# Kernel tuning notes

Measured on AMD Instinct MI355X. Metric: run time of the kernel, lower is better.

Reference implementation:

```python
import jax, jax.numpy as jnp
import numpy as np

N_NODES = 50000
N_EDGES = 800000
NODE_IN = 16
NODE_OUT = 3
H = 128
N_LAYERS = 3


def setup_inputs() -> dict:
    key = jax.random.key(0)
    ks = jax.random.split(key, 16)
    s = 0.05
    inp = {
        "x": jax.random.normal(ks[0], (N_NODES, NODE_IN), dtype=jnp.float32),
        "edge_index": jax.random.randint(ks[1], (2, N_EDGES), 0, N_NODES, dtype=jnp.int64),
        # encoder / decoder
        "enc_w": jax.random.normal(ks[2], (NODE_IN, H), dtype=jnp.float32) * s,
        "enc_b": jnp.zeros((H,), dtype=jnp.float32),
        "dec_w": jax.random.normal(ks[3], (H, NODE_OUT), dtype=jnp.float32) * s,
        "dec_b": jnp.zeros((NODE_OUT,), dtype=jnp.float32),
        # 3 processor layers, edge MLP: Linear(2H,H) -> ReLU -> Linear(H,H)
        "edge_w1": jax.random.normal(ks[4], (N_LAYERS, 2 * H, H), dtype=jnp.float32) * s,
        "edge_b1": jnp.zeros((N_LAYERS, H), dtype=jnp.float32),
        "edge_w2": jax.random.normal(ks[5], (N_LAYERS, H, H), dtype=jnp.float32) * s,
        "edge_b2": jnp.zeros((N_LAYERS, H), dtype=jnp.float32),
        # node MLP: Linear(2H,H) -> ReLU -> Linear(H,H)
        "node_w1": jax.random.normal(ks[6], (N_LAYERS, 2 * H, H), dtype=jnp.float32) * s,
        "node_b1": jnp.zeros((N_LAYERS, H), dtype=jnp.float32),
        "node_w2": jax.random.normal(ks[7], (N_LAYERS, H, H), dtype=jnp.float32) * s,
        "node_b2": jnp.zeros((N_LAYERS, H), dtype=jnp.float32),
    }
    return inp


def reference(x, edge_index, enc_w, enc_b, dec_w, dec_b,
              edge_w1, edge_b1, edge_w2, edge_b2,
              node_w1, node_b1, node_w2, node_b2):
    row = edge_index[0]  # source nodes
    col = edge_index[1]  # destination nodes
    h = x @ enc_w + enc_b  # [N, H]
    for l in range(N_LAYERS):
        # EdgeModel: cat(src, dest) -> MLP
        e_in = jnp.concatenate([h[row], h[col]], axis=1)  # [E, 2H]
        e = jnp.maximum(e_in @ edge_w1[l] + edge_b1[l], 0.0) @ edge_w2[l] + edge_b2[l]  # [E, H]
        # NodeModel: scatter_add messages by col, cat with x -> MLP
        agg = jax.ops.segment_sum(e, col, num_segments=h.shape[0])  # [N, H]
        n_in = jnp.concatenate([h, agg], axis=1)  # [N, 2H]
        h_upd = jnp.maximum(n_in @ node_w1[l] + node_b1[l], 0.0) @ node_w2[l] + node_b2[l]
        h = h + h_upd  # residual
    return h @ dec_w + dec_b  # [N, NODE_OUT]
```

## Files before the change

### kernel.cpp

```cpp
#include <hip/hip_runtime.h>
#include <hip/hip_bf16.h>
#include <stdint.h>

#define N_NODES 50000
#define N_EDGES 800000
#define HID 128
#define NODE_IN 16
#define NODE_OUT 3
#define EDGE_TILES 12500
#define NODE_TILES 782
#define SCAN_BLOCKS 196

typedef __attribute__((ext_vector_type(8))) short short8;
typedef __attribute__((ext_vector_type(4))) float f32x4;

__device__ __forceinline__ unsigned short f2bf(float f) {
    union { float f; unsigned int u; } v; v.f = f;
    unsigned int u = v.u;
    u += 0x7fff + ((u >> 16) & 1);
    return (unsigned short)(u >> 16);
}
__device__ __forceinline__ float bf2f(unsigned short s) {
    union { unsigned int u; float f; } v; v.u = ((unsigned int)s) << 16;
    return v.f;
}
__device__ __forceinline__ float bfu_lo(unsigned int u) {
    union { unsigned int u; float f; } v; v.u = u << 16; return v.f;
}
__device__ __forceinline__ float bfu_hi(unsigned int u) {
    union { unsigned int u; float f; } v; v.u = u & 0xffff0000u; return v.f;
}

__global__ void k1_hist_mfold(const int* __restrict__ colp, int* __restrict__ cnt,
                              int* __restrict__ rank,
                              const float* __restrict__ edge_w2, const float* __restrict__ node_w1,
                              const float* __restrict__ edge_b2,
                              float* __restrict__ Mtmp, float* __restrict__ Vtmp) {
    for (int e = blockIdx.x * 256 + threadIdx.x; e < N_EDGES; e += gridDim.x * 256)
        rank[e] = atomicAdd(&cnt[colp[e]], 1);
    for (int d = blockIdx.x * 256 + threadIdx.x; d < 3 * 16384; d += gridDim.x * 256) {
        int L = d / 16384, rem = d & 16383;
        int k = rem >> 7, n = rem & 127;
        const float* w2  = edge_w2 + (size_t)L * 16384;
        const float* w1b = node_w1 + (size_t)L * 32768 + 16384;
        float acc = 0.f;
        #pragma unroll 4
        for (int j = 0; j < 128; j++) acc += w2[k * 128 + j] * w1b[j * 128 + n];
        Mtmp[d] = acc;
        if (k == 0) {
            const float* b2 = edge_b2 + (size_t)L * 128;
            float vv = 0.f;
            #pragma unroll 4
            for (int j = 0; j < 128; j++) vv += b2[j] * w1b[j * 128 + n];
            Vtmp[L * 128 + n] = vv;
        }
    }
}

__global__ __launch_bounds__(256) void k2a_scan1_swizzle(
    const int* __restrict__ cnt, int* __restrict__ ex, int* __restrict__ bsums,
    const float* __restrict__ edge_w1, const float* __restrict__ node_w1,
    const float* __restrict__ node_w2, const float* __restrict__ Mtmp,
    unsigned short* __restrict__ swz) {
    __shared__ int s[256];
    int b = blockIdx.x, t = threadIdx.x;
    if (b < SCAN_BLOCKS) {
        int i = b * 256 + t;
        int v = (i < N_NODES) ? cnt[i] : 0;
        s[t] = v;
        __syncthreads();
        for (int off = 1; off < 256; off <<= 1) {
            int u = (t >= off) ? s[t - off] : 0;
            __syncthreads();
            s[t] += u;
            __syncthreads();
        }
        if (i < N_NODES) ex[i] = s[t] - v;
        if (t == 255) bsums[b] = s[255];
    } else {
        for (int d = (b - SCAN_BLOCKS) * 256 + t; d < 3 * 98304;
             d += (gridDim.x - SCAN_BLOCKS) * 256) {
            int L = d / 98304;
            int rem = d - L * 98304;
            unsigned short* base = swz + L * 98304;
            if (rem < 32768) {
                const float* w1 = edge_w1 + (size_t)L * 32768;
                int j = rem & 7, ll = (rem >> 3) & 63, tt = rem >> 9;
                int nt = tt & 15, kt = tt >> 4;
                int k = kt * 32 + ((ll >> 4) << 3) + j;
                int cc = nt * 16 + (ll & 15);
                float v = (cc < 128) ? w1[k * 128 + cc] : w1[(128 + k) * 128 + (cc - 128)];
                base[rem] = f2bf(v);
            } else if (rem < 49152) {
            } else if (rem < 81920) {
                int d2 = rem - 49152;
                int j = d2 & 7, ll = (d2 >> 3) & 63, tt = d2 >> 9;
                int nt = tt & 7, kt = tt >> 3;
                int k = kt * 32 + ((ll >> 4) << 3) + j, n = (nt << 4) + (ll & 15);
                float v = (k < 128) ? node_w1[(size_t)L * 32768 + k * 128 + n]
                                    : Mtmp[(size_t)L * 16384 + (k - 128) * 128 + n];
                base[rem] = f2bf(v);
            } else {
                int d2 = rem - 81920;
                const float* src = node_w2 + (size_t)L * 16384;
                int j = d2 & 7, ll = (d2 >> 3) & 63, tt = d2 >> 9;
                int nt = tt & 7, kt = tt >> 3;
                int k = kt * 32 + ((ll >> 4) << 3) + j, n = (nt << 4) + (ll & 15);
                base[rem] = f2bf(src[k * 128 + n]);
            }
        }
    }
}

__global__ __launch_bounds__(256) void k3a_scatter(
    const int* __restrict__ rowp, const int* __restrict__ colp,
    const int* __restrict__ ex, const int* __restrict__ bsums,
    const int* __restrict__ rank, int2* __restrict__ rc_sorted) {
    __shared__ int sc[256];
    __shared__ int ls[SCAN_BLOCKS];
    int t = threadIdx.x;
    int v = (t < SCAN_BLOCKS) ? bsums[t] : 0;
    sc[t] = v;
    __syncthreads();
    for (int off = 1; off < 256; off <<= 1) {
        int u = (t >= off) ? sc[t - off] : 0;
        __syncthreads();
        sc[t] += u;
        __syncthreads();
    }
    if (t < SCAN_BLOCKS) ls[t] = sc[t] - v;
    __syncthreads();

    int e = blockIdx.x * 256 + t;
    if (e >= N_EDGES) return;
    int c = colp[e];
    int pos = ex[c] + ls[c >> 8] + rank[e];
    rc_sorted[pos] = make_int2(rowp[e], c);
}

__global__ __launch_bounds__(256, 4) void k3b_encoder_sd(
    const float* __restrict__ x, const float* __restrict__ enc_w, const float* __restrict__ enc_b,
    const unsigned short* __restrict__ w1c, unsigned short* __restrict__ h,
    unsigned short* __restrict__ S, unsigned short* __restrict__ D, float* __restrict__ aggH)
{
    __shared__ float wts[NODE_IN * HID];
    __shared__ float bts[HID];
    __shared__ float xs[64][NODE_IN];
    __shared__ unsigned short hs[64][136];
    int t = threadIdx.x, wave = t >> 6, l = t & 63, q = l >> 4, l16 = l & 15;
    int n0 = blockIdx.x * 64;
    int nt0s = wave * 4;

    for (int i = t; i < NODE_IN * HID; i += 256) wts[i] = enc_w[i];
    if (t < HID) bts[t] = enc_b[t];
    for (int i = t; i < 64 * NODE_IN; i += 256) {
        int nl = i >> 4, ii = i & 15;
        int n = n0 + nl;
        xs[nl][ii] = (n < N_NODES) ? x[n * NODE_IN + ii] : 0.f;
    }
    for (int o = t; o < 64 * 32; o += 256) {
        int nl = o >> 5, c4 = o & 31;
        int n = n0 + nl;
        if (n < N_NODES) *(f32x4*)&aggH[n * HID + c4 * 4] = (f32x4){0.f, 0.f, 0.f, 0.f};
    }
    short8 wr[4][4];
    #pragma unroll
    for (int kt = 0; kt < 4; kt++)
        #pragma unroll
        for (int i = 0; i < 4; i++)
            wr[kt][i] = *(const short8*)(w1c + ((kt * 16 + nt0s + i) * 64 + l) * 8);
    __syncthreads();

    for (int o = t; o < 64 * HID; o += 256) {
        int nl = o >> 7, cc = o & 127;
        float acc = bts[cc];
        #pragma unroll
        for (int i = 0; i < NODE_IN; i++) acc += xs[nl][i] * wts[i * HID + cc];
        unsigned short hb = f2bf(acc);
        hs[nl][cc] = hb;
        int n = n0 + nl;
        if (n < N_NODES) h[n * HID + cc] = hb;
    }
    __syncthreads();

    f32x4 acc[4][4];
    #pragma unroll
    for (int g = 0; g < 4; g++)
        #pragma unroll
        for (int i = 0; i < 4; i++) acc[g][i] = (f32x4){0.f, 0.f, 0.f, 0.f};
    #pragma unroll
    for (int kt = 0; kt < 4; kt++) {
        #pragma unroll
        for (int g = 0; g < 4; g++) {
            short8 a = *(const short8*)&hs[g * 16 + l16][kt * 32 + q * 8];
            #pragma unroll
            for (int i = 0; i < 4; i++)
                acc[g][i] = __builtin_amdgcn_mfma_f32_16x16x32_bf16(a, wr[kt][i], acc[g][i], 0, 0, 0);
        }
    }
    #pragma unroll
    for (int i = 0; i < 4; i++) {
        int cc = (nt0s + i) * 16 + l16;
        #pragma unroll
        for (int g = 0; g < 4; g++)
            #pragma unroll
            for (int r = 0; r < 4; r++) {
                int n = n0 + g * 16 + q * 4 + r;
                if (n < N_NODES) {
                    unsigned short v = f2bf(acc[g][i][r]);
                    if (cc < 128) S[n * HID + cc] = v;
                    else          D[n * HID + (cc - 128)] = v;
                }
            }
    }
}

__global__ __launch_bounds__(256, 8) void edge_kernel(
    const unsigned short* __restrict__ S, const unsigned short* __restrict__ D,
    const int2* __restrict__ rc_sorted,
    const float* __restrict__ b1, float* __restrict__ aggH)
{
    __shared__ unsigned short hid_s[64][136];
    __shared__ int row_s[64], col_s[64];
    int t = threadIdx.x;
    int ch = t & 15;

    float b1v[8];
    #pragma unroll
    for (int j = 0; j < 8; j++) b1v[j] = b1[ch * 8 + j];

    for (int tile = blockIdx.x; tile < EDGE_TILES; tile += gridDim.x) {
        int e0 = tile * 64;
        if (t < 64) {
            int2 rc = rc_sorted[e0 + t];
            row_s[t] = rc.x;
            col_s[t] = rc.y;
        }
        __syncthreads();

        #pragma unroll
        for (int it = 0; it < 4; it++) {
            int el = it * 16 + (t >> 4);
            int r = row_s[el], c = col_s[el];
            short8 sv = *(const short8*)(S + (size_t)r * HID + ch * 8);
            short8 dv = *(const short8*)(D + (size_t)c * HID + ch * 8);
            short8 o;
            #pragma unroll
            for (int p = 0; p < 4; p++) {
                unsigned int us = ((const unsigned int*)&sv)[p];
                unsigned int ud = ((const unsigned int*)&dv)[p];
                float v0 = bfu_lo(us) + bfu_lo(ud) + b1v[p * 2];
                float v1 = bfu_hi(us) + bfu_hi(ud) + b1v[p * 2 + 1];
                ((unsigned short*)&o)[p * 2]     = f2bf(v0 > 0.f ? v0 : 0.f);
                ((unsigned short*)&o)[p * 2 + 1] = f2bf(v1 > 0.f ? v1 : 0.f);
            }
            *(short8*)&hid_s[el][ch * 8] = o;
        }
        __syncthreads();

        {
            int c = t & 127;
            int h2 = t >> 7;
            int r0 = h2 * 32;
            float accv = 0.f;
            int cur = col_s[r0];
            #pragma unroll 4
            for (int r = r0; r < r0 + 32; r++) {
                accv += bf2f(hid_s[r][c]);
                int nxt = (r == r0 + 31) ? -1 : col_s[r + 1];
                if (nxt != cur) {
                    unsafeAtomicAdd(&aggH[cur * HID + c], accv);
                    accv = 0.f;
                    cur = nxt;
                }
            }
        }
        __syncthreads();
    }
}

template<int LAST>
__global__ __launch_bounds__(256, 4) void node_kernel(
    unsigned short* __restrict__ h, float* __restrict__ aggH, const int* __restrict__ cnt,
    const unsigned short* __restrict__ w1m_s, const float* __restrict__ b1,
    const float* __restrict__ vfold,
    const unsigned short* __restrict__ w2s, const float* __restrict__ b2,
    const unsigned short* __restrict__ w1c_next,
    unsigned short* __restrict__ S, unsigned short* __restrict__ D,
    const float* __restrict__ dec_w, const float* __restrict__ dec_b, float* __restrict__ out)
{
    __shared__ unsigned short in_h[64][136];
    __shared__ unsigned short in_a[64][136];
    __shared__ int cnt_s[64];
    __shared__ float dw[HID * NODE_OUT];
    __shared__ float db[NODE_OUT];
    int t = threadIdx.x, wave = t >> 6, l = t & 63, q = l >> 4, l16 = l & 15;
    int nt0 = wave * 2, nt0s = wave * 4;
    int n0 = blockIdx.x * 64;

    if (LAST) {
        for (int i = t; i < HID * NODE_OUT; i += 256) dw[i] = dec_w[i];
        if (t < NODE_OUT) db[t] = dec_b[t];
    }

    #pragma unroll
    for (int it = 0; it < 8; it++) {
        int g = it * 256 + t;
        int nl = g >> 5, sub = g & 31, half = sub >> 4, li = sub & 15;
        int n = n0 + nl;
        short8 v = (short8){0, 0, 0, 0, 0, 0, 0, 0};
        if (n < N_NODES) {
            if (half == 0) {
                v = *(const short8*)(h + n * HID + li * 8);
            } else {
                float* ap = aggH + n * HID + li * 8;
                f32x4 a0 = *(f32x4*)ap, a1 = *(f32x4*)(ap + 4);
                #pragma unroll
                for (int j = 0; j < 4; j++) {
                    ((unsigned short*)&v)[j]     = f2bf(a0[j]);
                    ((unsigned short*)&v)[4 + j] = f2bf(a1[j]);
                }
                if (!LAST) {
                    *(f32x4*)ap       = (f32x4){0.f, 0.f, 0.f, 0.f};
                    *(f32x4*)(ap + 4) = (f32x4){0.f, 0.f, 0.f, 0.f};
                }
            }
        }
        if (half == 0) *(short8*)&in_h[nl][li * 8] = v;
        else           *(short8*)&in_a[nl][li * 8] = v;
    }
    if (t < 64) cnt_s[t] = (n0 + t < N_NODES) ? cnt[n0 + t] : 0;
    __syncthreads();

    float b1r0 = b1[nt0 * 16 + l16], b1r1 = b1[(nt0 + 1) * 16 + l16];
    float vr0 = vfold[nt0 * 16 + l16], vr1 = vfold[(nt0 + 1) * 16 + l16];
    float b2r0 = b2[nt0 * 16 + l16], b2r1 = b2[(nt0 + 1) * 16 + l16];

    f32x4 acc[4][2];
    #pragma unroll
    for (int g = 0; g < 4; g++)
        #pragma unroll
        for (int j = 0; j < 2; j++) acc[g][j] = (f32x4){0.f, 0.f, 0.f, 0.f};
    #pragma unroll
    for (int kt = 0; kt < 8; kt++) {
        short8 b0 = *(const short8*)(w1m_s + ((kt * 8 + nt0)     * 64 + l) * 8);
        short8 b1v = *(const short8*)(w1m_s + ((kt * 8 + nt0 + 1) * 64 + l) * 8);
        #pragma unroll
        for (int g = 0; g < 4; g++) {
            short8 a = (kt < 4) ? *(const short8*)&in_h[g * 16 + l16][kt * 32 + q * 8]
                                : *(const short8*)&in_a[g * 16 + l16][(kt - 4) * 32 + q * 8];
            acc[g][0] = __builtin_amdgcn_mfma_f32_16x16x32_bf16(a, b0, acc[g][0], 0, 0, 0);
            acc[g][1] = __builtin_amdgcn_mfma_f32_16x16x32_bf16(a, b1v, acc[g][1], 0, 0, 0);
        }
    }
    __syncthreads();

    #pragma unroll
    for (int j = 0; j < 2; j++) {
        float bv = j ? b1r1 : b1r0;
        float vv = j ? vr1 : vr0;
        #pragma unroll
        for (int g = 0; g < 4; g++)
            #pragma unroll
            for (int r = 0; r < 4; r++) {
                int m2 = g * 16 + q * 4 + r;
                float v = acc[g][j][r] + bv + (float)cnt_s[m2] * vv;
                v = v > 0.f ? v : 0.f;
                in_a[m2][(nt0 + j) * 16 + l16] = f2bf(v);
            }
    }
    __syncthreads();

    f32x4 acc2[4][2];
    #pragma unroll
    for (int g = 0; g < 4; g++)
        #pragma unroll
        for (int j = 0; j < 2; j++) acc2[g][j] = (f32x4){0.f, 0.f, 0.f, 0.f};
    #pragma unroll
    for (int kt = 0; kt < 4; kt++) {
        short8 b0 = *(const short8*)(w2s + ((kt * 8 + nt0)     * 64 + l) * 8);
        short8 b1v = *(const short8*)(w2s + ((kt * 8 + nt0 + 1) * 64 + l) * 8);
        #pragma unroll
        for (int g = 0; g < 4; g++) {
            short8 a = *(const short8*)&in_a[g * 16 + l16][kt * 32 + q * 8];
            acc2[g][0] = __builtin_amdgcn_mfma_f32_16x16x32_bf16(a, b0, acc2[g][0], 0, 0, 0);
            acc2[g][1] = __builtin_amdgcn_mfma_f32_16x16x32_bf16(a, b1v, acc2[g][1], 0, 0, 0);
        }
    }
    #pragma unroll
    for (int j = 0; j < 2; j++) {
        float bv = j ? b2r1 : b2r0;
        #pragma unroll
        for (int g = 0; g < 4; g++)
            #pragma unroll
            for (int r = 0; r < 4; r++) {
                float v = acc2[g][j][r] + bv;
                int m2 = g * 16 + q * 4 + r;
                int n = n0 + m2;
                if (n < N_NODES) {
                    int c = (nt0 + j) * 16 + l16;
                    unsigned short nh = f2bf(bf2f(in_h[m2][c]) + v);
                    if (!LAST) h[n * HID + c] = nh;
                    in_h[m2][c] = nh;
                }
            }
    }
    __syncthreads();

    if (!LAST) {
        #pragma unroll
        for (int p = 0; p < 2; p++) {
            short8 wr[4][2];
            #pragma unroll
            for (int kt = 0; kt < 4; kt++) {
                wr[kt][0] = *(const short8*)(w1c_next + ((kt * 16 + nt0s + p * 2)     * 64 + l) * 8);
                wr[kt][1] = *(const short8*)(w1c_next + ((kt * 16 + nt0s + p * 2 + 1) * 64 + l) * 8);
            }
            f32x4 accs[4][2];
            #pragma unroll
            for (int g = 0; g < 4; g++)
                #pragma unroll
                for (int i = 0; i < 2; i++) accs[g][i] = (f32x4){0.f, 0.f, 0.f, 0.f};
            #pragma unroll
            for (int kt = 0; kt < 4; kt++) {
                #pragma unroll
                for (int g = 0; g < 4; g++) {
                    short8 a = *(const short8*)&in_h[g * 16 + l16][kt * 32 + q * 8];
                    accs[g][0] = __builtin_amdgcn_mfma_f32_16x16x32_bf16(a, wr[kt][0], accs[g][0], 0, 0, 0);
                    accs[g][1] = __builtin_amdgcn_mfma_f32_16x16x32_bf16(a, wr[kt][1], accs[g][1], 0, 0, 0);
                }
            }
            #pragma unroll
            for (int i = 0; i < 2; i++) {
                int c = (nt0s + p * 2 + i) * 16 + l16;
                #pragma unroll
                for (int g = 0; g < 4; g++)
                    #pragma unroll
                    for (int r = 0; r < 4; r++) {
                        int n = n0 + g * 16 + q * 4 + r;
                        if (n < N_NODES) {
                            unsigned short v = f2bf(accs[g][i][r]);
                            if (c < 128) S[n * HID + c] = v;
                            else         D[n * HID + (c - 128)] = v;
                        }
                    }
            }
        }
    } else {
        if (t < 64 * NODE_OUT) {
            int nl = t / 3, o = t - 3 * nl;
            int n = n0 + nl;
            if (n < N_NODES) {
                float a = db[o];
                #pragma unroll 4
                for (int k = 0; k < HID; k++) a += bf2f(in_h[nl][k]) * dw[k * 3 + o];
                out[n * 3 + o] = a;
            }
        }
    }
}

extern "C" void kernel_launch(void* const* d_in, const int* in_sizes, int n_in,
                              void* d_out, int out_size, void* d_ws, size_t ws_size,
                              hipStream_t stream) {
    const float* x       = (const float*)d_in[0];
    const int*   ei      = (const int*)d_in[1];
    const float* enc_w   = (const float*)d_in[2];
    const float* enc_b   = (const float*)d_in[3];
    const float* dec_w   = (const float*)d_in[4];
    const float* dec_b   = (const float*)d_in[5];
    const float* edge_w1 = (const float*)d_in[6];
    const float* edge_b1 = (const float*)d_in[7];
    const float* edge_w2 = (const float*)d_in[8];
    const float* edge_b2 = (const float*)d_in[9];
    const float* node_w1 = (const float*)d_in[10];
    const float* node_b1 = (const float*)d_in[11];
    const float* node_w2 = (const float*)d_in[12];
    const float* node_b2 = (const float*)d_in[13];

    char* ws = (char*)d_ws;
    unsigned short* h    = (unsigned short*)ws;
    float*          aggH = (float*)(ws + 12800000);
    unsigned short* swz  = (unsigned short*)(ws + 38400000);
    int* cnt             = (int*)(ws + 38989824);
    int* ex              = (int*)(ws + 39189824);
    int* bsums           = (int*)(ws + 39389824);
    int2* rc_sorted      = (int2*)(ws + 39390848);
    unsigned short* Sbuf = (unsigned short*)(ws + 45790848);
    unsigned short* Dbuf = (unsigned short*)(ws + 58590848);
    float* Mtmp          = (float*)(ws + 71390848);
    float* Vtmp          = (float*)(ws + 71587456);
    int* rank            = (int*)(ws + 58590848);

    const int* rowp = ei;
    const int* colp = ei + N_EDGES;

    hipMemsetAsync(cnt, 0, (size_t)N_NODES * 4, stream);

    k1_hist_mfold<<<1024, 256, 0, stream>>>(colp, cnt, rank, edge_w2, node_w1, edge_b2,
                                            Mtmp, Vtmp);
    k2a_scan1_swizzle<<<SCAN_BLOCKS + 288, 256, 0, stream>>>(cnt, ex, bsums, edge_w1,
                                                             node_w1, node_w2, Mtmp, swz);
    k3a_scatter<<<3125, 256, 0, stream>>>(rowp, colp, ex, bsums, rank, rc_sorted);
    k3b_encoder_sd<<<NODE_TILES, 256, 0, stream>>>(x, enc_w, enc_b, swz , h,
                                                   Sbuf, Dbuf, aggH);

    for (int L = 0; L < 3; L++) {
        unsigned short* base = swz + (size_t)L * 98304;
        unsigned short* next = swz + (size_t)(L + 1) * 98304;
        edge_kernel<<<2048, 256, 0, stream>>>(Sbuf, Dbuf, rc_sorted,
                                              edge_b1 + (size_t)L * HID, aggH);
        if (L < 2) {
            node_kernel<0><<<NODE_TILES, 256, 0, stream>>>(
                h, aggH, cnt,
                base + 49152, node_b1 + (size_t)L * HID, Vtmp + (size_t)L * HID,
                base + 81920, node_b2 + (size_t)L * HID,
                next, Sbuf, Dbuf, dec_w, dec_b, (float*)d_out);
        } else {
            node_kernel<1><<<NODE_TILES, 256, 0, stream>>>(
                h, aggH, cnt,
                base + 49152, node_b1 + (size_t)L * HID, Vtmp + (size_t)L * HID,
                base + 81920, node_b2 + (size_t)L * HID,
                base , Sbuf, Dbuf, dec_w, dec_b, (float*)d_out);
        }
    }
}
```

Before: 389.7 us.

## Make edge kernel wave-local, fold edge bias into D precompute, use packed bf16 convert

The edge kernel now has each 64-lane wave own 16 edges of the tile for gather, ReLU and segmented reduction, so the block-wide __syncthreads barriers become wave-local waits. The edge bias b1 is folded into the precomputed D projection in the encoder and node kernels, which removes per-edge bias adds. Scalar bf16 rounding is replaced with the hardware v_cvt_pk_bf16_f32 instruction. Each lane now reduces two channels over 16 edges instead of one channel over 32, so atomics happen in shorter segments and may increase in count.

Result: slower. 543.1 us (+39.4%).

```diff
diff --git a/kernel.cpp b/kernel.cpp
--- a/kernel.cpp
+++ b/kernel.cpp
@@ -13,6 +13,7 @@
 
 typedef __attribute__((ext_vector_type(8))) short short8;
 typedef __attribute__((ext_vector_type(4))) float f32x4;
+typedef __attribute__((ext_vector_type(4))) unsigned int u32x4;
 
 __device__ __forceinline__ unsigned short f2bf(float f) {
     union { float f; unsigned int u; } v; v.f = f;
@@ -29,6 +30,11 @@
 }
 __device__ __forceinline__ float bfu_hi(unsigned int u) {
     union { unsigned int u; float f; } v; v.u = u & 0xffff0000u; return v.f;
+}
+__device__ __forceinline__ unsigned int cvt_pk_bf16(float lo, float hi) {
+    unsigned int r;
+    asm("v_cvt_pk_bf16_f32 %0, %1, %2" : "=v"(r) : "v"(lo), "v"(hi));
+    return r;
 }
 
 __global__ void k1_hist_mfold(const int* __restrict__ colp, int* __restrict__ cnt,
@@ -140,7 +146,8 @@
 
 __global__ __launch_bounds__(256, 4) void k3b_encoder_sd(
     const float* __restrict__ x, const float* __restrict__ enc_w, const float* __restrict__ enc_b,
-    const unsigned short* __restrict__ w1c, unsigned short* __restrict__ h,
+    const unsigned short* __restrict__ w1c, const float* __restrict__ eb1,
+    unsigned short* __restrict__ h,
     unsigned short* __restrict__ S, unsigned short* __restrict__ D, float* __restrict__ aggH)
 {
     __shared__ float wts[NODE_IN * HID];
@@ -201,13 +208,15 @@
     #pragma unroll
     for (int i = 0; i < 4; i++) {
         int cc = (nt0s + i) * 16 + l16;
+        float badd = 0.f;
+        if (cc >= 128) badd = eb1[cc - 128];
         #pragma unroll
         for (int g = 0; g < 4; g++)
             #pragma unroll
             for (int r = 0; r < 4; r++) {
                 int n = n0 + g * 16 + q * 4 + r;
                 if (n < N_NODES) {
-                    unsigned short v = f2bf(acc[g][i][r]);
+                    unsigned short v = f2bf(acc[g][i][r] + badd);
                     if (cc < 128) S[n * HID + cc] = v;
                     else          D[n * HID + (cc - 128)] = v;
                 }
@@ -217,65 +226,67 @@
 
 __global__ __launch_bounds__(256, 8) void edge_kernel(
     const unsigned short* __restrict__ S, const unsigned short* __restrict__ D,
-    const int2* __restrict__ rc_sorted,
-    const float* __restrict__ b1, float* __restrict__ aggH)
+    const int2* __restrict__ rc_sorted, float* __restrict__ aggH)
 {
     __shared__ unsigned short hid_s[64][136];
     __shared__ int row_s[64], col_s[64];
     int t = threadIdx.x;
-    int ch = t & 15;
-
-    float b1v[8];
-    #pragma unroll
-    for (int j = 0; j < 8; j++) b1v[j] = b1[ch * 8 + j];
+    int l = t & 63, w = t >> 6;
+    int ch = l & 15, eg = l >> 4;
+    int rbase = w * 16;
 
     for (int tile = blockIdx.x; tile < EDGE_TILES; tile += gridDim.x) {
-        int e0 = tile * 64;
-        if (t < 64) {
-            int2 rc = rc_sorted[e0 + t];
-            row_s[t] = rc.x;
-            col_s[t] = rc.y;
-        }
-        __syncthreads();
+        int e0 = tile * 64 + rbase;
+        if (l < 16) {
+            int2 rc = rc_sorted[e0 + l];
+            row_s[rbase + l] = rc.x;
+            col_s[rbase + l] = rc.y;
+        }
+        asm volatile("s_waitcnt lgkmcnt(0)" ::: "memory");
+        __builtin_amdgcn_sched_barrier(0);
 
         #pragma unroll
         for (int it = 0; it < 4; it++) {
-            int el = it * 16 + (t >> 4);
+            int el = rbase + it * 4 + eg;
             int r = row_s[el], c = col_s[el];
             short8 sv = *(const short8*)(S + (size_t)r * HID + ch * 8);
             short8 dv = *(const short8*)(D + (size_t)c * HID + ch * 8);
-            short8 o;
+            u32x4 o;
             #pragma unroll
             for (int p = 0; p < 4; p++) {
                 unsigned int us = ((const unsigned int*)&sv)[p];
                 unsigned int ud = ((const unsigned int*)&dv)[p];
-                float v0 = bfu_lo(us) + bfu_lo(ud) + b1v[p * 2];
-                float v1 = bfu_hi(us) + bfu_hi(ud) + b1v[p * 2 + 1];
-                ((unsigned short*)&o)[p * 2]     = f2bf(v0 > 0.f ? v0 : 0.f);
-                ((unsigned short*)&o)[p * 2 + 1] = f2bf(v1 > 0.f ? v1 : 0.f);
-            }
-            *(short8*)&hid_s[el][ch * 8] = o;
-        }
-        __syncthreads();
-
-        {
-            int c = t & 127;
-            int h2 = t >> 7;
-            int r0 = h2 * 32;
-            float accv = 0.f;
-            int cur = col_s[r0];
-            #pragma unroll 4
-            for (int r = r0; r < r0 + 32; r++) {
-                accv += bf2f(hid_s[r][c]);
-                int nxt = (r == r0 + 31) ? -1 : col_s[r + 1];
-                if (nxt != cur) {
-                    unsafeAtomicAdd(&aggH[cur * HID + c], accv);
-                    accv = 0.f;
-                    cur = nxt;
-                }
-            }
-        }
-        __syncthreads();
+                float v0 = bfu_lo(us) + bfu_lo(ud);
+                float v1 = bfu_hi(us) + bfu_hi(ud);
+                v0 = v0 > 0.f ? v0 : 0.f;
+                v1 = v1 > 0.f ? v1 : 0.f;
+                o[p] = cvt_pk_bf16(v0, v1);
+            }
+            *(u32x4*)&hid_s[el][ch * 8] = o;
+        }
+        asm volatile("s_waitcnt lgkmcnt(0)" ::: "memory");
+        __builtin_amdgcn_sched_barrier(0);
+
+        int cols[16];
+        *(int4*)&cols[0]  = *(const int4*)&col_s[rbase + 0];
+        *(int4*)&cols[4]  = *(const int4*)&col_s[rbase + 4];
+        *(int4*)&cols[8]  = *(const int4*)&col_s[rbase + 8];
+        *(int4*)&cols[12] = *(const int4*)&col_s[rbase + 12];
+        float a0 = 0.f, a1 = 0.f;
+        int cur = cols[0];
+        #pragma unroll
+        for (int i = 0; i < 16; i++) {
+            unsigned int u = *(const unsigned int*)&hid_s[rbase + i][l * 2];
+            a0 += bfu_lo(u);
+            a1 += bfu_hi(u);
+            int nxt = (i == 15) ? -1 : cols[i + 1];
+            if (nxt != cur) {
+                unsafeAtomicAdd(&aggH[(size_t)cur * HID + l * 2], a0);
+                unsafeAtomicAdd(&aggH[(size_t)cur * HID + l * 2 + 1], a1);
+                a0 = 0.f; a1 = 0.f;
+                cur = nxt;
+            }
+        }
     }
 }
 
@@ -285,7 +296,7 @@
     const unsigned short* __restrict__ w1m_s, const float* __restrict__ b1,
     const float* __restrict__ vfold,
     const unsigned short* __restrict__ w2s, const float* __restrict__ b2,
-    const unsigned short* __restrict__ w1c_next,
+    const unsigned short* __restrict__ w1c_next, const float* __restrict__ eb1n,
     unsigned short* __restrict__ S, unsigned short* __restrict__ D,
     const float* __restrict__ dec_w, const float* __restrict__ dec_b, float* __restrict__ out)
 {
@@ -315,11 +326,11 @@
             } else {
                 float* ap = aggH + n * HID + li * 8;
                 f32x4 a0 = *(f32x4*)ap, a1 = *(f32x4*)(ap + 4);
-                #pragma unroll
-                for (int j = 0; j < 4; j++) {
-                    ((unsigned short*)&v)[j]     = f2bf(a0[j]);
-                    ((unsigned short*)&v)[4 + j] = f2bf(a1[j]);
-                }
+                unsigned int* vp = (unsigned int*)&v;
+                vp[0] = cvt_pk_bf16(a0[0], a0[1]);
+                vp[1] = cvt_pk_bf16(a0[2], a0[3]);
+                vp[2] = cvt_pk_bf16(a1[0], a1[1]);
+                vp[3] = cvt_pk_bf16(a1[2], a1[3]);
                 if (!LAST) {
                     *(f32x4*)ap       = (f32x4){0.f, 0.f, 0.f, 0.f};
                     *(f32x4*)(ap + 4) = (f32x4){0.f, 0.f, 0.f, 0.f};
@@ -433,13 +444,15 @@
             #pragma unroll
             for (int i = 0; i < 2; i++) {
                 int c = (nt0s + p * 2 + i) * 16 + l16;
+                float badd = 0.f;
+                if (c >= 128) badd = eb1n[c - 128];
                 #pragma unroll
                 for (int g = 0; g < 4; g++)
                     #pragma unroll
                     for (int r = 0; r < 4; r++) {
                         int n = n0 + g * 16 + q * 4 + r;
                         if (n < N_NODES) {
-                            unsigned short v = f2bf(accs[g][i][r]);
+                            unsigned short v = f2bf(accs[g][i][r] + badd);
                             if (c < 128) S[n * HID + c] = v;
                             else         D[n * HID + (c - 128)] = v;
                         }
@@ -502,26 +515,26 @@
     k2a_scan1_swizzle<<<SCAN_BLOCKS + 288, 256, 0, stream>>>(cnt, ex, bsums, edge_w1,
                                                              node_w1, node_w2, Mtmp, swz);
     k3a_scatter<<<3125, 256, 0, stream>>>(rowp, colp, ex, bsums, rank, rc_sorted);
-    k3b_encoder_sd<<<NODE_TILES, 256, 0, stream>>>(x, enc_w, enc_b, swz , h,
+    k3b_encoder_sd<<<NODE_TILES, 256, 0, stream>>>(x, enc_w, enc_b, swz ,
+                                                   edge_b1 , h,
                                                    Sbuf, Dbuf, aggH);
 
     for (int L = 0; L < 3; L++) {
         unsigned short* base = swz + (size_t)L * 98304;
         unsigned short* next = swz + (size_t)(L + 1) * 98304;
-        edge_kernel<<<2048, 256, 0, stream>>>(Sbuf, Dbuf, rc_sorted,
-                                              edge_b1 + (size_t)L * HID, aggH);
+        edge_kernel<<<2048, 256, 0, stream>>>(Sbuf, Dbuf, rc_sorted, aggH);
         if (L < 2) {
             node_kernel<0><<<NODE_TILES, 256, 0, stream>>>(
                 h, aggH, cnt,
                 base + 49152, node_b1 + (size_t)L * HID, Vtmp + (size_t)L * HID,
                 base + 81920, node_b2 + (size_t)L * HID,
-                next, Sbuf, Dbuf, dec_w, dec_b, (float*)d_out);
+                next, edge_b1 + (size_t)(L + 1) * HID, Sbuf, Dbuf, dec_w, dec_b, (float*)d_out);
         } else {
             node_kernel<1><<<NODE_TILES, 256, 0, stream>>>(
                 h, aggH, cnt,
                 base + 49152, node_b1 + (size_t)L * HID, Vtmp + (size_t)L * HID,
                 base + 81920, node_b2 + (size_t)L * HID,
-                base , Sbuf, Dbuf, dec_w, dec_b, (float*)d_out);
-        }
-    }
-}
+                base , edge_b1 , Sbuf, Dbuf, dec_w, dec_b, (float*)d_out);
+        }
+    }
+}
```
